# Kernel tuning notes

Hardware: AMD Instinct MI355X
Metric: run time of the kernel (lower is better)

The kernel has to match this reference:

```python
import jax, jax.numpy as jnp
import numpy as np

N_NEIGHBORS = 200
OUT_HW = 64

def avg_pool3(x):
    # F.avg_pool2d(x, 3, stride=1, padding=1), count_include_pad=True -> divide by 9
    s = jax.lax.reduce_window(x, 0.0, jax.lax.add, (1, 1, 3, 3), (1, 1, 1, 1),
                              ((0, 0), (0, 0), (1, 1), (1, 1)))
    return s / 9.0

def coord_conv1x1(x, w, b):
    # CoordConv2d: append normalized x/y coord channels in [-1,1], then 1x1 conv.
    B, C, H, W = x.shape
    yy = jnp.linspace(-1.0, 1.0, H, dtype=x.dtype)
    xx = jnp.linspace(-1.0, 1.0, W, dtype=x.dtype)
    xg = jnp.broadcast_to(xx[None, :], (H, W))
    yg = jnp.broadcast_to(yy[:, None], (H, W))
    coords = jnp.broadcast_to(jnp.stack([xg, yg])[None], (B, 2, H, W))
    xc = jnp.concatenate([x, coords], axis=1)  # (B, C+2, H, W)
    return jnp.einsum('bchw,oc->bohw', xc, w) + b[None, :, None, None]

def resize64(x):
    B, C, _, _ = x.shape
    return jax.image.resize(x, (B, C, OUT_HW, OUT_HW), method='bilinear')

def descriptor(p0, p1, p2, w1, b1, w2, b2, w3, b3):
    o1 = resize64(coord_conv1x1(avg_pool3(p0), w1, b1))
    o2 = resize64(coord_conv1x1(avg_pool3(p1), w2, b2))
    o3 = resize64(coord_conv1x1(avg_pool3(p2), w3, b3))
    return jnp.concatenate([o1, o2, o3], axis=1)  # (B, 1792, 64, 64)

def setup_inputs() -> dict:
    key = jax.random.key(0)
    ks = jax.random.split(key, 10)
    s = 0.05
    return {
        'p0': jax.random.normal(ks[0], (4, 256, 64, 64), jnp.float32),
        'p1': jax.random.normal(ks[1], (4, 512, 32, 32), jnp.float32),
        'p2': jax.random.normal(ks[2], (4, 1024, 16, 16), jnp.float32),
        'label': 0,
        'mask': jnp.ones((4, 1, 64, 64), jnp.float32),
        'w1': jax.random.normal(ks[3], (256, 258), jnp.float32) * s,
        'b1': jax.random.normal(ks[4], (256,), jnp.float32) * s,
        'w2': jax.random.normal(ks[5], (512, 514), jnp.float32) * s,
        'b2': jax.random.normal(ks[6], (512,), jnp.float32) * s,
        'w3': jax.random.normal(ks[7], (1024, 1026), jnp.float32) * s,
        'b3': jax.random.normal(ks[8], (1024,), jnp.float32) * s,
        'C': jax.random.normal(ks[9], (1792, 4096), jnp.float32),
    }

def reference(p0, p1, p2, label, mask, w1, b1, w2, b2, w3, b3, C):
    PHI_P = descriptor(p0, p1, p2, w1, b1, w2, b2, w3, b3)  # (B, 1792, 64, 64)
    B = PHI_P.shape[0]
    # b c h w -> b (h w) c
    phi_p = PHI_P.reshape(B, 1792, OUT_HW * OUT_HW).transpose(0, 2, 1)  # (B, 4096, 1792)
    feats = jnp.sum(phi_p * phi_p, axis=2, keepdims=True)       # (B, 4096, 1)
    cents = jnp.sum(C * C, axis=0, keepdims=True)                # (1, 4096)
    f_c = 2.0 * jnp.matmul(phi_p, C)                             # (B, 4096, 4096)
    dist = jnp.sqrt(feats + cents - f_c)
    # topk smallest: top_k on negated distances, sorted ascending after negation
    neg_vals, _ = jax.lax.top_k(-dist, N_NEIGHBORS)              # (B, 4096, 200)
    score = -neg_vals
    # b (h w) c -> b c h w
    score = score.reshape(B, OUT_HW, OUT_HW, N_NEIGHBORS).transpose(0, 3, 1, 2)
    return (score, PHI_P[:, :896, :, :])
```

## Files before the change

### kernel.cpp

```cpp
#include <hip/hip_runtime.h>
#include <hip/hip_bf16.h>
#include <hip/hip_fp8.h>
#include <stdint.h>

typedef unsigned short u16;
typedef __attribute__((ext_vector_type(8))) short bf16x8;
typedef __attribute__((ext_vector_type(4))) unsigned short u16x4;
typedef __attribute__((ext_vector_type(4))) float f32x4;

#define AS1 __attribute__((address_space(1)))
#define AS3 __attribute__((address_space(3)))

__device__ __forceinline__ u16 f2bf(float f) {
  uint32_t x = __float_as_uint(f);
  uint32_t r = (x + 0x7FFFu + ((x >> 16) & 1u)) >> 16;
  return (u16)r;
}
__device__ __forceinline__ float bf2f(u16 u) {
  return __uint_as_float(((uint32_t)u) << 16);
}
__device__ __forceinline__ uint8_t f2f8(float f) {
  __hip_fp8_e4m3 t(f);
  return (uint8_t)t.__x;
}
__device__ __forceinline__ float f82f(uint8_t v) {
  __hip_fp8_e4m3 t;
  t.__x = (__hip_fp8_storage_t)v;
  return (float)t;
}

__device__ __forceinline__ void gload_lds16(const void* g, void* l) {
  __builtin_amdgcn_global_load_lds((const AS1 void*)g, (AS3 void*)l, 16, 0, 0);
}

template <int C, int H, int W>
__global__ __launch_bounds__(256) void pool_trans(const float* __restrict__ in,
                                                  u16* __restrict__ PT) {
  constexpr int HW = H * W;
  int hwt = blockIdx.x, ct = blockIdx.y, b = blockIdx.z;
  int tid = threadIdx.x;
  __shared__ float t[32][33];
  {
    int c_l = tid >> 3;
    int hw_l = (tid & 7) * 4;
    int c = ct * 32 + c_l;
    int hw = hwt * 32 + hw_l;
    int y = hw / W;
    int x0 = hw % W;
    const float* pl = in + ((size_t)b * C + c) * HW;
    float cs[6] = {0, 0, 0, 0, 0, 0};
    #pragma unroll
    for (int dy = -1; dy <= 1; dy++) {
      int yy = y + dy;
      if ((unsigned)yy < (unsigned)H) {
        const float* row = pl + yy * W;
        #pragma unroll
        for (int k = 0; k < 6; k++) {
          int xx = x0 - 1 + k;
          if ((unsigned)xx < (unsigned)W) cs[k] += row[xx];
        }
      }
    }
    #pragma unroll
    for (int k = 0; k < 4; k++)
      t[c_l][hw_l + k] = (cs[k] + cs[k + 1] + cs[k + 2]) * (1.0f / 9.0f);
  }
  __syncthreads();
  int hw_w = tid >> 3;
  int c_w = (tid & 7) * 4;
  u16x4 o;
  #pragma unroll
  for (int j = 0; j < 4; j++) o[j] = f2bf(t[c_w + j][hw_w]);
  *(u16x4*)&PT[((size_t)b * HW + hwt * 32 + hw_w) * C + ct * 32 + c_w] = o;
}

__global__ void wconv_bf16(const float* __restrict__ wf, u16* __restrict__ wb,
                           int logk, int total) {
  int idx = blockIdx.x * 256 + threadIdx.x;
  if (idx >= total) return;
  int K = 1 << logk;
  int o = idx >> (logk - 3);
  int k0 = (idx & ((K >> 3) - 1)) * 8;
  const float* src = wf + (size_t)o * (K + 2) + k0;
  bf16x8 v;
  #pragma unroll
  for (int e = 0; e < 8; e++) v[e] = (short)f2bf(src[e]);
  *(bf16x8*)&wb[(size_t)o * K + k0] = v;
}

template <int K, int HW, int WD, int OC, int PHIC, int CST, bool OUT8>
__global__ __launch_bounds__(256) void conv_gemm(
    const u16* __restrict__ Wb,
    const u16* __restrict__ PT,
    const float* __restrict__ wf,
    const float* __restrict__ bias,
    float* __restrict__ outHW, size_t outHW_bstride,
    void* __restrict__ outCM) {
  constexpr int LOGW = (WD == 64) ? 6 : (WD == 32) ? 5 : 4;
  constexpr int LOGHW = 2 * LOGW;
  int n0 = blockIdx.x * 128, m0 = blockIdx.y * 128;
  int tid = threadIdx.x;
  int wid = tid >> 6, lane = tid & 63;
  int wm = wid >> 1, wn = wid & 1;
  __shared__ u16 As[128 * 64];
  __shared__ u16 Bs[128 * 64];
  f32x4 acc[4][4] = {};
  int lrow = tid >> 3;
  int lcol = (tid & 7) * 8;
  const u16* ga = Wb + (size_t)(m0 + lrow) * K + lcol;
  const u16* gb = PT + (size_t)(n0 + lrow) * K + lcol;
  char* lbaseA = (char*)As + wid * 1024;
  char* lbaseB = (char*)Bs + wid * 1024;
  for (int k0 = 0; k0 < K; k0 += 64) {
    #pragma unroll
    for (int q = 0; q < 4; q++) {
      gload_lds16(ga + (size_t)q * 32 * K + k0, lbaseA + q * 4096);
      gload_lds16(gb + (size_t)q * 32 * K + k0, lbaseB + q * 4096);
    }
    __syncthreads();
    #pragma unroll
    for (int kk = 0; kk < 2; kk++) {
      bf16x8 af[4], bfr[4];
      int kb = kk * 32 + (lane >> 4) * 8;
      #pragma unroll
      for (int i = 0; i < 4; i++)
        af[i] = *(const bf16x8*)&As[(wm * 64 + i * 16 + (lane & 15)) * 64 + kb];
      #pragma unroll
      for (int j = 0; j < 4; j++)
        bfr[j] = *(const bf16x8*)&Bs[(wn * 64 + j * 16 + (lane & 15)) * 64 + kb];
      #pragma unroll
      for (int i = 0; i < 4; i++)
        #pragma unroll
        for (int j = 0; j < 4; j++)
          acc[i][j] = __builtin_amdgcn_mfma_f32_16x16x32_bf16(af[i], bfr[j], acc[i][j], 0, 0, 0);
    }
    __syncthreads();
  }
  int rq = lane >> 4, cq = lane & 15;
  #pragma unroll
  for (int mi = 0; mi < 4; mi++) {
    int lm = m0 + wm * 64 + mi * 16 + rq * 4;
    float wxr[4], wyr[4], bbr[4];
    #pragma unroll
    for (int r = 0; r < 4; r++) {
      int o = lm + r;
      wxr[r] = wf[(size_t)o * (K + 2) + K];
      wyr[r] = wf[(size_t)o * (K + 2) + K + 1];
      bbr[r] = bias[o];
    }
    #pragma unroll
    for (int ni = 0; ni < 4; ni++) {
      int gn = n0 + wn * 64 + ni * 16 + cq;
      int b = gn >> LOGHW;
      int hw = gn & (HW - 1);
      int x = hw & (WD - 1), y = hw >> LOGW;
      float xg = -1.0f + x * (2.0f / (WD - 1));
      float yg = -1.0f + y * (2.0f / (WD - 1));
      float vals[4];
      #pragma unroll
      for (int r = 0; r < 4; r++)
        vals[r] = acc[mi][ni][r] + wxr[r] * xg + wyr[r] * yg + bbr[r];
      if (lm < PHIC) {
        #pragma unroll
        for (int r = 0; r < 4; r++)
          outHW[(size_t)b * outHW_bstride + (size_t)(lm + r) * HW + hw] = vals[r];
      }
      if constexpr (OUT8) {
        uint32_t pk = (uint32_t)f2f8(vals[0]) | ((uint32_t)f2f8(vals[1]) << 8) |
                      ((uint32_t)f2f8(vals[2]) << 16) | ((uint32_t)f2f8(vals[3]) << 24);
        *(uint32_t*)&((uint8_t*)outCM)[((size_t)b * HW + hw) * CST + lm] = pk;
      } else {
        u16x4 pk;
        #pragma unroll
        for (int r = 0; r < 4; r++) pk[r] = f2bf(vals[r]);
        *(u16x4*)&((u16*)outCM)[((size_t)b * HW + hw) * CST + lm] = pk;
      }
    }
  }
}

template <int Hin>
__device__ __forceinline__ void bilin_coords(int v, int& i0, int& i1, float& wgt) {
  constexpr float scale = (float)Hin / 64.0f;
  float f = ((float)v + 0.5f) * scale - 0.5f;
  float f0 = floorf(f);
  wgt = f - f0;
  int i = (int)f0;
  i1 = min(i + 1, Hin - 1);
  i0 = max(i, 0);
}

template <int C, int Cin, int Hin>
__global__ void emit_phi_v(const float* __restrict__ in, float* __restrict__ outp,
                           int ch_off) {
  int idx = blockIdx.x * 256 + threadIdx.x;
  int x0 = (idx & 15) * 4;
  int y = (idx >> 4) & 63;
  int c = (idx >> 10) % C;
  int b = idx / (C * 1024);
  const float* pl = in + (size_t)(b * Cin + c) * (Hin * Hin);
  int y0, y1; float wy;
  bilin_coords<Hin>(y, y0, y1, wy);
  const float* r0 = pl + y0 * Hin;
  const float* r1 = pl + y1 * Hin;
  f32x4 o;
  #pragma unroll
  for (int k = 0; k < 4; k++) {
    int xx0, xx1; float wx;
    bilin_coords<Hin>(x0 + k, xx0, xx1, wx);
    float top = (1.0f - wx) * r0[xx0] + wx * r0[xx1];
    float bot = (1.0f - wx) * r1[xx0] + wx * r1[xx1];
    o[k] = (1.0f - wy) * top + wy * bot;
  }
  *(f32x4*)&outp[((size_t)b * 896 + ch_off + c) * 4096 + (y << 6) + x0] = o;
}

__global__ __launch_bounds__(256) void trans_f32_fp8(
    const float* __restrict__ in, uint8_t* __restrict__ outT, int R, int Cc, int OS) {
  int r0 = blockIdx.y * 32, c0 = blockIdx.x * 32;
  __shared__ float t[32][33];
  int tid = threadIdx.x;
  int cl = tid & 31, rl = tid >> 5;
  #pragma unroll
  for (int q = 0; q < 4; q++)
    t[rl + q * 8][cl] = in[(size_t)(r0 + rl + q * 8) * Cc + c0 + cl];
  __syncthreads();
  #pragma unroll
  for (int q = 0; q < 4; q++) {
    int c = c0 + rl + q * 8;
    outT[(size_t)c * OS + r0 + cl] = f2f8(t[cl][rl + q * 8]);
  }
}

template <int C, int Hin, int L>
__global__ void gather_A(const u16* __restrict__ OT, uint8_t* __restrict__ A,
                         int ch_off) {
  int idx = blockIdx.x * 256 + threadIdx.x;
  int co = (idx & ((C / 8) - 1)) * 8;
  int hw = (idx >> L) & 4095;
  int b = idx >> (L + 12);
  int x = hw & 63, y = hw >> 6;
  int y0, y1, x0, x1; float wy, wx;
  bilin_coords<Hin>(y, y0, y1, wy);
  bilin_coords<Hin>(x, x0, x1, wx);
  float w00 = (1.0f - wy) * (1.0f - wx), w01 = (1.0f - wy) * wx;
  float w10 = wy * (1.0f - wx), w11 = wy * wx;
  const u16* base = OT + (size_t)b * (Hin * Hin) * C + co;
  bf16x8 t00 = *(const bf16x8*)&base[(y0 * Hin + x0) * C];
  bf16x8 t01 = *(const bf16x8*)&base[(y0 * Hin + x1) * C];
  bf16x8 t10 = *(const bf16x8*)&base[(y1 * Hin + x0) * C];
  bf16x8 t11 = *(const bf16x8*)&base[(y1 * Hin + x1) * C];
  uint32_t pk[2] = {0, 0};
  #pragma unroll
  for (int e = 0; e < 8; e++) {
    float v = w00 * bf2f((u16)t00[e]) + w01 * bf2f((u16)t01[e]) +
              w10 * bf2f((u16)t10[e]) + w11 * bf2f((u16)t11[e]);
    pk[e >> 2] |= ((uint32_t)f2f8(v)) << ((e & 3) * 8);
  }
  uint2 o; o.x = pk[0]; o.y = pk[1];
  *(uint2*)&A[((size_t)b * 4096 + hw) * 1792 + ch_off + co] = o;
}

__global__ __launch_bounds__(256) void rownorm8(const uint8_t* __restrict__ X,
                                                float* __restrict__ out, int ncols) {
  int row = blockIdx.x * 4 + (threadIdx.x >> 6);
  int lane = threadIdx.x & 63;
  const uint8_t* xr = X + (size_t)row * ncols;
  int n8 = ncols >> 3;
  float s = 0.0f;
  for (int c8 = lane; c8 < n8; c8 += 64) {
    uint2 v = *(const uint2*)&xr[c8 * 8];
    #pragma unroll
    for (int e = 0; e < 4; e++) {
      float f = f82f((uint8_t)((v.x >> (8 * e)) & 0xFF));
      s = fmaf(f, f, s);
    }
    #pragma unroll
    for (int e = 0; e < 4; e++) {
      float f = f82f((uint8_t)((v.y >> (8 * e)) & 0xFF));
      s = fmaf(f, f, s);
    }
  }
  #pragma unroll
  for (int off = 32; off; off >>= 1) s += __shfl_down(s, off);
  if (lane == 0) out[row] = s;
}

#define GD_NT 28

__device__ __forceinline__ void stage8k64(const uint8_t* __restrict__ G, int row0,
                                          int k0, char* lds_wavebase, int lane) {
  const int K = 1792;
  int sub = lane >> 2;
  int colsw = 16 * ((lane & 3) ^ ((lane >> 3) & 3));
  #pragma unroll
  for (int q = 0; q < 2; q++) {
    gload_lds16(G + (size_t)(row0 + q * 128 + sub) * K + k0 + colsw,
                lds_wavebase + q * 8192);
  }
}

__global__ __launch_bounds__(512, 2) void gemm_dist2(
    const uint8_t* __restrict__ A,
    const uint8_t* __restrict__ Bt,
    const float* __restrict__ feats, const float* __restrict__ cents,
    u16* __restrict__ S16, int m_base) {
  const int K = 1792, N = 4096;
  extern __shared__ uint8_t lds8[];
  int bid = blockIdx.x;
  int swz = (bid & 7) * 32 + (bid >> 3);
  int m0 = (swz >> 4) * 256;
  int n0 = (swz & 15) * 256;
  int tid = threadIdx.x;
  int wid = tid >> 6, lane = tid & 63;
  int wr = wid >> 2, wc = wid & 3;
  int ln15 = lane & 15;
  int sl = lane >> 4;
  int key = (ln15 >> 1) & 3;
  int fo0 = ((((sl >> 1)) ^ key) << 4) | ((sl & 1) << 3);
  int fo1 = (((2 + (sl >> 1)) ^ key) << 4) | ((sl & 1) << 3);

  f32x4 acc[8][4] = {};

  #pragma unroll
  for (int t = 0; t < 3; t++) {
    char* bufb = (char*)lds8 + (t & 3) * 32768 + wid * 1024;
    stage8k64(A, m_base + m0 + wid * 16, t * 64, bufb, lane);
    stage8k64(Bt, n0 + wid * 16, t * 64, bufb + 16384, lane);
  }

  #pragma unroll 1
  for (int t = 0; t < GD_NT; t++) {
    asm volatile("s_waitcnt vmcnt(8)" ::: "memory");
    __builtin_amdgcn_s_barrier();
    __builtin_amdgcn_sched_barrier(0);
    const uint8_t* Ab = lds8 + (t & 3) * 32768;
    const uint8_t* Bb = Ab + 16384;
    char* nbuf = (char*)lds8 + ((t + 3) & 3) * 32768 + wid * 1024;

    {
      long bq[4], af[8];
      #pragma unroll
      for (int ni = 0; ni < 4; ni++)
        bq[ni] = *(const long*)&Bb[(wc * 64 + ni * 16 + ln15) * 64 + fo0];
      #pragma unroll
      for (int mi = 0; mi < 8; mi++)
        af[mi] = *(const long*)&Ab[(wr * 128 + mi * 16 + ln15) * 64 + fo0];
      if (t + 3 < GD_NT) stage8k64(A, m_base + m0 + wid * 16, (t + 3) * 64, nbuf, lane);
      __builtin_amdgcn_s_setprio(1);
      #pragma unroll
      for (int mi = 0; mi < 8; mi++)
        #pragma unroll
        for (int ni = 0; ni < 4; ni++)
          acc[mi][ni] = __builtin_amdgcn_mfma_f32_16x16x32_fp8_fp8(af[mi], bq[ni], acc[mi][ni], 0, 0, 0);
      __builtin_amdgcn_s_setprio(0);
    }
    {
      long bq[4], af[8];
      #pragma unroll
      for (int ni = 0; ni < 4; ni++)
        bq[ni] = *(const long*)&Bb[(wc * 64 + ni * 16 + ln15) * 64 + fo1];
      #pragma unroll
      for (int mi = 0; mi < 8; mi++)
        af[mi] = *(const long*)&Ab[(wr * 128 + mi * 16 + ln15) * 64 + fo1];
      if (t + 3 < GD_NT) stage8k64(Bt, n0 + wid * 16, (t + 3) * 64, nbuf + 16384, lane);
      __builtin_amdgcn_s_setprio(1);
      #pragma unroll
      for (int mi = 0; mi < 8; mi++)
        #pragma unroll
        for (int ni = 0; ni < 4; ni++)
          acc[mi][ni] = __builtin_amdgcn_mfma_f32_16x16x32_fp8_fp8(af[mi], bq[ni], acc[mi][ni], 0, 0, 0);
      __builtin_amdgcn_s_setprio(0);
    }
  }

  int rq = lane >> 4, cq = lane & 15;
  #pragma unroll
  for (int mi = 0; mi < 8; mi++) {
    int lm = m0 + wr * 128 + mi * 16 + rq * 4;
    #pragma unroll
    for (int ni = 0; ni < 4; ni++) {
      int gn = n0 + wc * 64 + ni * 16 + cq;
      float cn = cents[gn];
      #pragma unroll
      for (int r = 0; r < 4; r++)
        S16[(size_t)(lm + r) * N + gn] =
            f2bf(feats[m_base + lm + r] + cn - 2.0f * acc[mi][ni][r]);
    }
  }
}

__global__ __launch_bounds__(256) void select_topk(const u16* __restrict__ S16,
                                                   float* __restrict__ out,
                                                   int row_base) {
  int wv = threadIdx.x >> 6, lane = threadIdx.x & 63;
  int row_local = blockIdx.x * 4 + wv;
  const u16* Sr = S16 + (size_t)row_local * 4096;
  uint32_t ku[64];
  #pragma unroll
  for (int g = 0; g < 8; g++) {
    bf16x8 v = *(const bf16x8*)&Sr[g * 512 + lane * 8];
    #pragma unroll
    for (int e = 0; e < 8; e++) {
      uint32_t u = (uint32_t)(u16)v[e];
      u ^= (u & 0x8000u) ? 0xFFFFu : 0x8000u;
      ku[g * 8 + e] = u;
    }
  }
  uint32_t mn = 0xFFFFu, mx = 0u;
  #pragma unroll
  for (int j = 0; j < 64; j++) {
    mn = min(mn, ku[j]);
    mx = max(mx, ku[j]);
  }
  #pragma unroll
  for (int off = 1; off < 64; off <<= 1) {
    mn = min(mn, (uint32_t)__shfl_xor((int)mn, off));
    mx = max(mx, (uint32_t)__shfl_xor((int)mx, off));
  }
  uint32_t lo = mn, hi = mx;
  while (lo < hi) {
    uint32_t mid = (lo + hi) >> 1;
    int c = 0;
    #pragma unroll
    for (int j = 0; j < 64; j++) c += (ku[j] <= mid) ? 1 : 0;
    #pragma unroll
    for (int off = 1; off < 64; off <<= 1) c += __shfl_xor(c, off);
    if (c >= 200) hi = mid; else lo = mid + 1;
  }
  uint32_t T = lo;
  int cl = 0;
  #pragma unroll
  for (int j = 0; j < 64; j++) cl += (ku[j] < T) ? 1 : 0;
  int incl = cl;
  #pragma unroll
  for (int off = 1; off < 64; off <<= 1) {
    int v = __shfl_up(incl, off);
    if (lane >= off) incl += v;
  }
  int nless = __shfl(incl, 63);
  int pos = incl - cl;
  __shared__ uint32_t selv[4][256];
  uint32_t* sv = selv[wv];
  #pragma unroll
  for (int g = 0; g < 4; g++) sv[g * 64 + lane] = 0xFFFFFFFFu;
  for (int p = nless + lane; p < 200; p += 64) sv[p] = T;
  #pragma unroll
  for (int j = 0; j < 64; j++)
    if (ku[j] < T) sv[pos++] = ku[j];
  uint32_t v[4];
  #pragma unroll
  for (int q = 0; q < 4; q++) v[q] = sv[q * 64 + lane];
  #pragma unroll
  for (int kk = 2; kk <= 256; kk <<= 1) {
    #pragma unroll
    for (int jj = kk >> 1; jj > 0; jj >>= 1) {
      if (jj >= 64) {
        int qb = jj >> 6;
        #pragma unroll
        for (int q = 0; q < 4; q++) {
          if ((q & qb) == 0) {
            int q2 = q | qb;
            bool up = (kk == 256) ? true : ((q & (kk >> 6)) == 0);
            uint32_t a = v[q], b2 = v[q2];
            uint32_t lo2 = min(a, b2), hi2 = max(a, b2);
            v[q] = up ? lo2 : hi2;
            v[q2] = up ? hi2 : lo2;
          }
        }
      } else {
        #pragma unroll
        for (int q = 0; q < 4; q++) {
          bool up;
          if (kk == 256) up = true;
          else if (kk == 128) up = ((q & 2) == 0);
          else if (kk == 64) up = ((q & 1) == 0);
          else up = ((lane & kk) == 0);
          uint32_t other = (uint32_t)__shfl_xor((int)v[q], jj);
          bool lower = ((lane & jj) == 0);
          uint32_t lo2 = min(v[q], other), hi2 = max(v[q], other);
          v[q] = (up == lower) ? lo2 : hi2;
        }
      }
    }
  }
  int grow = row_base + row_local;
  int b = grow >> 12, r = grow & 4095;
  #pragma unroll
  for (int q = 0; q < 4; q++) {
    int i = q * 64 + lane;
    if (i < 200) {
      uint32_t u = v[q] & 0xFFFFu;
      u ^= (u & 0x8000u) ? 0x8000u : 0xFFFFu;
      out[((size_t)b * 200 + i) * 4096 + r] = sqrtf(bf2f((u16)u));
    }
  }
}

extern "C" void kernel_launch(void* const* d_in, const int* in_sizes, int n_in,
                              void* d_out, int out_size, void* d_ws, size_t ws_size,
                              hipStream_t stream) {
  const float* p0 = (const float*)d_in[0];
  const float* p1 = (const float*)d_in[1];
  const float* p2 = (const float*)d_in[2];
  const float* w1 = (const float*)d_in[5];
  const float* b1 = (const float*)d_in[6];
  const float* w2 = (const float*)d_in[7];
  const float* b2 = (const float*)d_in[8];
  const float* w3 = (const float*)d_in[9];
  const float* b3 = (const float*)d_in[10];
  const float* Cm = (const float*)d_in[11];

  float* out_score = (float*)d_out;
  float* out_phi = (float*)d_out + 3276800;

  char* w = (char*)d_ws;
  uint8_t* A8 = (uint8_t*)w;
  uint8_t* Ct8 = (uint8_t*)(w + 29360128);
  float* feats = (float*)(w + 36700160);
  float* cents = (float*)(w + 36765696);
  u16* S16 = (u16*)(w + 36782080);
  u16* PT1 = (u16*)(w + 36782080);
  u16* PT2 = (u16*)(w + 45170688);
  u16* PT3 = (u16*)(w + 49364992);
  u16* Wbf1 = (u16*)(w + 51462144);
  u16* Wbf2 = (u16*)(w + 51593216);
  u16* Wbf3 = (u16*)(w + 52117504);
  float* O2 = (float*)(w + 54214656);
  float* O3 = (float*)(w + 62603264);
  u16* OT2 = (u16*)(w + 63127552);
  u16* OT3 = (u16*)(w + 67321856);

  pool_trans<256, 64, 64><<<dim3(128, 8, 4), 256, 0, stream>>>(p0, PT1);
  pool_trans<512, 32, 32><<<dim3(32, 16, 4), 256, 0, stream>>>(p1, PT2);
  pool_trans<1024, 16, 16><<<dim3(8, 32, 4), 256, 0, stream>>>(p2, PT3);

  wconv_bf16<<<32, 256, 0, stream>>>(w1, Wbf1, 8, 8192);
  wconv_bf16<<<128, 256, 0, stream>>>(w2, Wbf2, 9, 32768);
  wconv_bf16<<<512, 256, 0, stream>>>(w3, Wbf3, 10, 131072);

  conv_gemm<256, 4096, 64, 256, 256, 1792, true><<<dim3(128, 2), 256, 0, stream>>>(
      Wbf1, PT1, w1, b1, out_phi, (size_t)896 * 4096, A8);
  conv_gemm<512, 1024, 32, 512, 512, 512, false><<<dim3(32, 4), 256, 0, stream>>>(
      Wbf2, PT2, w2, b2, O2, (size_t)512 * 1024, OT2);
  conv_gemm<1024, 256, 16, 1024, 128, 1024, false><<<dim3(8, 8), 256, 0, stream>>>(
      Wbf3, PT3, w3, b3, O3, (size_t)128 * 256, OT3);

  emit_phi_v<512, 512, 32><<<8192, 256, 0, stream>>>(O2, out_phi, 256);
  emit_phi_v<128, 128, 16><<<2048, 256, 0, stream>>>(O3, out_phi, 768);

  gather_A<512, 32, 6><<<4096, 256, 0, stream>>>(OT2, A8, 256);
  gather_A<1024, 16, 7><<<8192, 256, 0, stream>>>(OT3, A8, 768);

  trans_f32_fp8<<<dim3(128, 56), 256, 0, stream>>>(Cm, Ct8, 1792, 4096, 1792);

  rownorm8<<<4096, 256, 0, stream>>>(A8, feats, 1792);
  rownorm8<<<1024, 256, 0, stream>>>(Ct8, cents, 1792);

  for (int mc = 0; mc < 4; mc++) {
    gemm_dist2<<<256, 512, 131072, stream>>>(A8, Ct8, feats, cents, S16, mc * 4096);
    select_topk<<<1024, 256, 0, stream>>>(S16, out_score, mc * 4096);
  }
}
```

Measured before the change: 430.1 us.

## Permute fp8 K-column layout so GEMM fragments load with 16-byte LDS reads

```diff
diff --git a/kernel.cpp b/kernel.cpp
--- a/kernel.cpp
+++ b/kernel.cpp
@@ -7,6 +7,7 @@
 typedef __attribute__((ext_vector_type(8))) short bf16x8;
 typedef __attribute__((ext_vector_type(4))) unsigned short u16x4;
 typedef __attribute__((ext_vector_type(4))) float f32x4;
+typedef __attribute__((ext_vector_type(2))) long lx2;
 
 #define AS1 __attribute__((address_space(1)))
 #define AS3 __attribute__((address_space(3)))
@@ -27,6 +28,10 @@
   __hip_fp8_e4m3 t;
   t.__x = (__hip_fp8_storage_t)v;
   return (float)t;
+}
+
+__device__ __forceinline__ int permcol(int c) {
+  return (c & ~63) | (((c >> 3) & 3) << 4) | (((c >> 5) & 1) << 3) | (c & 7);
 }
 
 __device__ __forceinline__ void gload_lds16(const void* g, void* l) {
@@ -168,7 +173,7 @@
       if constexpr (OUT8) {
         uint32_t pk = (uint32_t)f2f8(vals[0]) | ((uint32_t)f2f8(vals[1]) << 8) |
                       ((uint32_t)f2f8(vals[2]) << 16) | ((uint32_t)f2f8(vals[3]) << 24);
-        *(uint32_t*)&((uint8_t*)outCM)[((size_t)b * HW + hw) * CST + lm] = pk;
+        *(uint32_t*)&((uint8_t*)outCM)[((size_t)b * HW + hw) * CST + permcol(lm)] = pk;
       } else {
         u16x4 pk;
         #pragma unroll
@@ -228,7 +233,7 @@
   #pragma unroll
   for (int q = 0; q < 4; q++) {
     int c = c0 + rl + q * 8;
-    outT[(size_t)c * OS + r0 + cl] = f2f8(t[cl][rl + q * 8]);
+    outT[(size_t)c * OS + permcol(r0 + cl)] = f2f8(t[cl][rl + q * 8]);
   }
 }
 
@@ -258,7 +263,7 @@
     pk[e >> 2] |= ((uint32_t)f2f8(v)) << ((e & 3) * 8);
   }
   uint2 o; o.x = pk[0]; o.y = pk[1];
-  *(uint2*)&A[((size_t)b * 4096 + hw) * 1792 + ch_off + co] = o;
+  *(uint2*)&A[((size_t)b * 4096 + hw) * 1792 + permcol(ch_off + co)] = o;
 }
 
 __global__ __launch_bounds__(256) void rownorm8(const uint8_t* __restrict__ X,
@@ -315,10 +320,7 @@
   int wid = tid >> 6, lane = tid & 63;
   int wr = wid >> 2, wc = wid & 3;
   int ln15 = lane & 15;
-  int sl = lane >> 4;
-  int key = (ln15 >> 1) & 3;
-  int fo0 = ((((sl >> 1)) ^ key) << 4) | ((sl & 1) << 3);
-  int fo1 = (((2 + (sl >> 1)) ^ key) << 4) | ((sl & 1) << 3);
+  int fo = 16 * ((lane >> 4) ^ ((lane >> 1) & 3));
 
   f32x4 acc[8][4] = {};
 
@@ -338,40 +340,31 @@
     const uint8_t* Bb = Ab + 16384;
     char* nbuf = (char*)lds8 + ((t + 3) & 3) * 32768 + wid * 1024;
 
-    {
-      long bq[4], af[8];
+    lx2 bq[4], af[8];
+    #pragma unroll
+    for (int ni = 0; ni < 4; ni++)
+      bq[ni] = *(const lx2*)&Bb[(wc * 64 + ni * 16 + ln15) * 64 + fo];
+    #pragma unroll
+    for (int mi = 0; mi < 8; mi++)
+      af[mi] = *(const lx2*)&Ab[(wr * 128 + mi * 16 + ln15) * 64 + fo];
+
+    if (t + 3 < GD_NT) {
+      stage8k64(A, m_base + m0 + wid * 16, (t + 3) * 64, nbuf, lane);
+      stage8k64(Bt, n0 + wid * 16, (t + 3) * 64, nbuf + 16384, lane);
+    }
+
+    __builtin_amdgcn_s_setprio(1);
+    #pragma unroll
+    for (int mi = 0; mi < 8; mi++)
       #pragma unroll
       for (int ni = 0; ni < 4; ni++)
-        bq[ni] = *(const long*)&Bb[(wc * 64 + ni * 16 + ln15) * 64 + fo0];
-      #pragma unroll
-      for (int mi = 0; mi < 8; mi++)
-        af[mi] = *(const long*)&Ab[(wr * 128 + mi * 16 + ln15) * 64 + fo0];
-      if (t + 3 < GD_NT) stage8k64(A, m_base + m0 + wid * 16, (t + 3) * 64, nbuf, lane);
-      __builtin_amdgcn_s_setprio(1);
-      #pragma unroll
-      for (int mi = 0; mi < 8; mi++)
-        #pragma unroll
-        for (int ni = 0; ni < 4; ni++)
-          acc[mi][ni] = __builtin_amdgcn_mfma_f32_16x16x32_fp8_fp8(af[mi], bq[ni], acc[mi][ni], 0, 0, 0);
-      __builtin_amdgcn_s_setprio(0);
-    }
-    {
-      long bq[4], af[8];
+        acc[mi][ni] = __builtin_amdgcn_mfma_f32_16x16x32_fp8_fp8(af[mi][0], bq[ni][0], acc[mi][ni], 0, 0, 0);
+    #pragma unroll
+    for (int mi = 0; mi < 8; mi++)
       #pragma unroll
       for (int ni = 0; ni < 4; ni++)
-        bq[ni] = *(const long*)&Bb[(wc * 64 + ni * 16 + ln15) * 64 + fo1];
-      #pragma unroll
-      for (int mi = 0; mi < 8; mi++)
-        af[mi] = *(const long*)&Ab[(wr * 128 + mi * 16 + ln15) * 64 + fo1];
-      if (t + 3 < GD_NT) stage8k64(Bt, n0 + wid * 16, (t + 3) * 64, nbuf + 16384, lane);
-      __builtin_amdgcn_s_setprio(1);
-      #pragma unroll
-      for (int mi = 0; mi < 8; mi++)
-        #pragma unroll
-        for (int ni = 0; ni < 4; ni++)
-          acc[mi][ni] = __builtin_amdgcn_mfma_f32_16x16x32_fp8_fp8(af[mi], bq[ni], acc[mi][ni], 0, 0, 0);
-      __builtin_amdgcn_s_setprio(0);
-    }
+        acc[mi][ni] = __builtin_amdgcn_mfma_f32_16x16x32_fp8_fp8(af[mi][1], bq[ni][1], acc[mi][ni], 0, 0, 0);
+    __builtin_amdgcn_s_setprio(0);
   }
 
   int rq = lane >> 4, cq = lane & 15;
```

Result: faster. 415.8 us (-3.3%).
